# Kernel tuning notes

Measured on AMD Instinct MI355X. Metric: run time of the kernel, lower is better.

## Reference

```python
import jax, jax.numpy as jnp
import numpy as np

B, V = 4096, 50257          # batch, command-logit width
NUM_CAT, CMDS_PER_CAT = 8, 8
TOTAL_CMDS = NUM_CAT * CMDS_PER_CAT  # sum(len(cmds)) in source
TOPK = 5                    # min(5, V)
W_CMD, W_CAT = 0.6, 0.4     # hierarchy_weights


def setup_inputs() -> dict:
    key = jax.random.key(0)
    k1, k2, k3 = jax.random.split(key, 3)
    logits = jax.random.normal(k1, (B, V), dtype=jnp.float32)
    labels = jax.random.randint(k2, (B,), 0, V)
    category_labels = jax.random.randint(k3, (B,), 0, NUM_CAT)
    # precomputed command -> category index table (replaces python range search)
    cmd_to_cat = jnp.asarray(np.repeat(np.arange(NUM_CAT), CMDS_PER_CAT), dtype=jnp.int32)
    return {"logits": logits, "labels": labels,
            "category_labels": category_labels, "cmd_to_cat": cmd_to_cat}


def _cross_entropy(logits, labels):
    # mean NLL, matching torch.nn.CrossEntropyLoss defaults
    logp = jax.nn.log_softmax(logits, axis=-1)
    nll = -jnp.take_along_axis(logp, labels[:, None], axis=-1)[:, 0]
    return jnp.mean(nll)


def reference(logits, labels, category_labels, cmd_to_cat):
    command_loss = _cross_entropy(logits, labels)

    # _aggregate_category_logits, vectorized:
    # topk values are exactly logits[b, cmd_idx] gathered in the source loop
    vals, idx = jax.lax.top_k(logits, TOPK)          # [B, K]
    cat_idx = cmd_to_cat[idx % TOTAL_CMDS]           # [B, K] category bins
    b = jnp.arange(logits.shape[0])[:, None]          # [B, 1]
    category_logits = jnp.zeros((logits.shape[0], NUM_CAT), dtype=logits.dtype)
    category_logits = category_logits.at[b, cat_idx].add(vals)

    category_loss = _cross_entropy(category_logits, category_labels)
    return W_CMD * command_loss + W_CAT * category_loss
```

## Files before the change

kernel.cpp:

```cpp
#include <hip/hip_runtime.h>
#include <math.h>

#define TPB 256
#define NCAT 8
#define LOG2E  1.44269504088896f
#define LN2    0.69314718055994f
#define SHIFT  32.0f

__global__ __launch_bounds__(TPB) void hcl_row_kernel(
    const float* __restrict__ logits,
    const int*   __restrict__ labels,
    const int*   __restrict__ cat_labels,
    const int*   __restrict__ cmd_to_cat,
    float*       __restrict__ row_loss,
    int V)
{
    const int row  = blockIdx.x;
    const int tid  = threadIdx.x;
    const int lane = tid & 63;
    const int wave = tid >> 6;
    const float* __restrict__ rl = logits + (size_t)row * (size_t)V;

    float s0 = 0.0f, s1 = 0.0f, s2 = 0.0f, s3 = 0.0f;
    float v0=-INFINITY, v1=-INFINITY, v2=-INFINITY, v3=-INFINITY, v4=-INFINITY;
    int   i0=0, i1=0, i2=0, i3=0, i4=0;

#define INSERT(val, gidx) do {                                               \
        v4 = (val); i4 = (gidx);                                             \
        if (v4 > v3) { float t=v3; v3=v4; v4=t; int u=i3; i3=i4; i4=u; }     \
        if (v3 > v2) { float t=v2; v2=v3; v3=t; int u=i2; i2=i3; i3=u; }     \
        if (v2 > v1) { float t=v1; v1=v2; v2=t; int u=i1; i1=i2; i2=u; }     \
        if (v1 > v0) { float t=v0; v0=v1; v1=t; int u=i0; i0=i1; i1=u; }     \
    } while (0)

    const int mis = (int)(((size_t)rl >> 2) & 3);
    const int pre = (4 - mis) & 3;
    const int nb  = (V - pre) >> 2;
    const float4* __restrict__ body = (const float4*)(rl + pre);

    for (int i = tid; i < nb; i += TPB) {
        float4 q = body[i];
        int gi = pre + 4 * i;
        s0 += exp2f(__builtin_fmaf(q.x, LOG2E, -SHIFT));
        s1 += exp2f(__builtin_fmaf(q.y, LOG2E, -SHIFT));
        s2 += exp2f(__builtin_fmaf(q.z, LOG2E, -SHIFT));
        s3 += exp2f(__builtin_fmaf(q.w, LOG2E, -SHIFT));
        if (__builtin_expect(q.x > v4, 0)) INSERT(q.x, gi);
        if (__builtin_expect(q.y > v4, 0)) INSERT(q.y, gi + 1);
        if (__builtin_expect(q.z > v4, 0)) INSERT(q.z, gi + 2);
        if (__builtin_expect(q.w > v4, 0)) INSERT(q.w, gi + 3);
    }
    if (tid < pre) {
        float v = rl[tid];
        s0 += exp2f(__builtin_fmaf(v, LOG2E, -SHIFT));
        if (v > v4) INSERT(v, tid);
    }
    for (int gi = pre + 4 * nb + tid; gi < V; gi += TPB) {
        float v = rl[gi];
        s0 += exp2f(__builtin_fmaf(v, LOG2E, -SHIFT));
        if (v > v4) INSERT(v, gi);
    }
#undef INSERT

    float s = (s0 + s1) + (s2 + s3);
    #pragma unroll
    for (int off = 32; off > 0; off >>= 1) s += __shfl_down(s, off);

    __shared__ float sh_s[TPB/64];
    __shared__ float sh_cv[TPB/64];
    __shared__ int   sh_ci[TPB/64];
    __shared__ float sh_bv;
    __shared__ int   sh_bi;

    if (lane == 0) sh_s[wave] = s;

    float top_v[5]; int top_i[5];
    #pragma unroll
    for (int r = 0; r < 5; ++r) {
        float cv = v0; int ci = i0;
        #pragma unroll
        for (int off = 32; off > 0; off >>= 1) {
            float ov = __shfl_down(cv, off);
            int   oi = __shfl_down(ci, off);
            if (ov > cv || (ov == cv && oi < ci)) { cv = ov; ci = oi; }
        }
        if (lane == 0) { sh_cv[wave] = cv; sh_ci[wave] = ci; }
        __syncthreads();
        if (tid == 0) {
            float bv = sh_cv[0]; int bi = sh_ci[0];
            #pragma unroll
            for (int w = 1; w < TPB/64; ++w) {
                float ov = sh_cv[w]; int oi = sh_ci[w];
                if (ov > bv || (ov == bv && oi < bi)) { bv = ov; bi = oi; }
            }
            sh_bv = bv; sh_bi = bi;
            top_v[r] = bv; top_i[r] = bi;
        }
        __syncthreads();
        if (v0 == sh_bv && i0 == sh_bi) {
            v0=v1; i0=i1; v1=v2; i1=i2; v2=v3; i2=i3; v3=v4; i3=i4;
            v4=-INFINITY; i4=0;
        }
    }

    if (tid == 0) {
        float fs = 0.0f;
        #pragma unroll
        for (int w = 0; w < TPB/64; ++w) fs += sh_s[w];
        float lse = (log2f(fs) + SHIFT) * LN2;
        float nll_cmd = lse - rl[labels[row]];

        float cl[NCAT];
        #pragma unroll
        for (int c = 0; c < NCAT; ++c) cl[c] = 0.0f;
        #pragma unroll
        for (int r = 0; r < 5; ++r) {
            int c = cmd_to_cat[top_i[r] & 63];
            float v = top_v[r];
            #pragma unroll
            for (int k = 0; k < NCAT; ++k)
                cl[k] += (k == c) ? v : 0.0f;
        }
        float mc = cl[0];
        #pragma unroll
        for (int c = 1; c < NCAT; ++c) mc = fmaxf(mc, cl[c]);
        float se = 0.0f;
        #pragma unroll
        for (int c = 0; c < NCAT; ++c) se += __expf(cl[c] - mc);
        float lsec = mc + __logf(se);

        int clab = cat_labels[row];
        float tgt = 0.0f;
        #pragma unroll
        for (int c = 0; c < NCAT; ++c) tgt += (c == clab) ? cl[c] : 0.0f;
        float nll_cat = lsec - tgt;

        row_loss[row] = 0.6f * nll_cmd + 0.4f * nll_cat;
    }
}

__global__ __launch_bounds__(TPB) void hcl_reduce_kernel(
    const float* __restrict__ row_loss, float* __restrict__ out, int B)
{
    const int tid = threadIdx.x;
    float s = 0.0f;
    for (int i = tid; i < B; i += TPB) s += row_loss[i];
    #pragma unroll
    for (int off = 32; off > 0; off >>= 1) s += __shfl_down(s, off);
    __shared__ float sh[TPB/64];
    const int lane = tid & 63, wave = tid >> 6;
    if (lane == 0) sh[wave] = s;
    __syncthreads();
    if (tid == 0) {
        float t = 0.0f;
        #pragma unroll
        for (int w = 0; w < TPB/64; ++w) t += sh[w];
        out[0] = t / (float)B;
    }
}

extern "C" void kernel_launch(void* const* d_in, const int* in_sizes, int n_in,
                              void* d_out, int out_size, void* d_ws, size_t ws_size,
                              hipStream_t stream) {
    const float* logits     = (const float*)d_in[0];
    const int*   labels     = (const int*)  d_in[1];
    const int*   cat_labels = (const int*)  d_in[2];
    const int*   cmd_to_cat = (const int*)  d_in[3];
    const int B = in_sizes[1];
    const int V = in_sizes[0] / B;
    float* row_loss = (float*)d_ws;

    hcl_row_kernel<<<B, TPB, 0, stream>>>(logits, labels, cat_labels,
                                          cmd_to_cat, row_loss, V);
    hcl_reduce_kernel<<<1, TPB, 0, stream>>>(row_loss, (float*)d_out, B);
}
```

Measured before the change: 1.069 ms.

## Replace per-thread top-5 insertion with threshold-filtered shared candidate list

The main streaming loop no longer keeps a per-thread sorted top-5. Values above a fixed threshold are appended to a shared candidate buffer through an atomic counter, and a single wave then picks the top 5 from that buffer. If fewer than 5 or more than CAP candidates are found, the kernel falls back to rescanning the row with the old insertion method. The loop is also unrolled to two float4 loads per iteration with eight accumulators. This removes branchy insertion work from the hot loop, but it depends on the input distribution, since the threshold assumes standard-normal logits, and the fallback pays for a second full read of the row.

Measured after the change: 1.031 ms. 3.6% less time.

```diff
diff --git a/kernel.cpp b/kernel.cpp
--- a/kernel.cpp
+++ b/kernel.cpp
@@ -3,6 +3,8 @@
 
 #define TPB 256
 #define NCAT 8
+#define CAP 512
+#define TAU 3.0f
 #define LOG2E  1.44269504088896f
 #define LN2    0.69314718055994f
 #define SHIFT  32.0f
@@ -21,10 +23,101 @@
     const int wave = tid >> 6;
     const float* __restrict__ rl = logits + (size_t)row * (size_t)V;
 
-    float s0 = 0.0f, s1 = 0.0f, s2 = 0.0f, s3 = 0.0f;
-    float v0=-INFINITY, v1=-INFINITY, v2=-INFINITY, v3=-INFINITY, v4=-INFINITY;
-    int   i0=0, i1=0, i2=0, i3=0, i4=0;
-
+    __shared__ float cand_v[CAP];
+    __shared__ int   cand_i[CAP];
+    __shared__ int   s_cnt;
+    __shared__ float sh_s[TPB/64];
+    __shared__ float s_top_v[5];
+    __shared__ int   s_top_i[5];
+    __shared__ int   s_c2c[64];
+    __shared__ float sh_cv[TPB/64];
+    __shared__ int   sh_ci[TPB/64];
+    __shared__ float sh_bv;
+    __shared__ int   sh_bi;
+
+    if (tid == 0) s_cnt = 0;
+    if (tid < 64) s_c2c[tid] = cmd_to_cat[tid];
+
+    int lab = 0, clab = 0; float tgt = 0.0f;
+    if (tid == 0) { lab = labels[row]; clab = cat_labels[row]; tgt = rl[lab]; }
+    __syncthreads();
+
+    const int mis = (int)(((size_t)rl >> 2) & 3);
+    const int pre = (4 - mis) & 3;
+    const int nb  = (V - pre) >> 2;
+    const float4* __restrict__ body = (const float4*)(rl + pre);
+
+    float a0=0.f,a1=0.f,a2=0.f,a3=0.f,a4=0.f,a5=0.f,a6=0.f,a7=0.f;
+
+#define APPEND(val, gidx) do {                                               \
+        int _s = atomicAdd(&s_cnt, 1);                                       \
+        if (_s < CAP) { cand_v[_s] = (val); cand_i[_s] = (gidx); }           \
+    } while (0)
+
+    int i = tid;
+    for (; i + TPB < nb; i += 2*TPB) {
+        float4 x = body[i];
+        float4 y = body[i + TPB];
+        a0 += exp2f(__builtin_fmaf(x.x, LOG2E, -SHIFT));
+        a1 += exp2f(__builtin_fmaf(x.y, LOG2E, -SHIFT));
+        a2 += exp2f(__builtin_fmaf(x.z, LOG2E, -SHIFT));
+        a3 += exp2f(__builtin_fmaf(x.w, LOG2E, -SHIFT));
+        a4 += exp2f(__builtin_fmaf(y.x, LOG2E, -SHIFT));
+        a5 += exp2f(__builtin_fmaf(y.y, LOG2E, -SHIFT));
+        a6 += exp2f(__builtin_fmaf(y.z, LOG2E, -SHIFT));
+        a7 += exp2f(__builtin_fmaf(y.w, LOG2E, -SHIFT));
+        float mx = fmaxf(fmaxf(fmaxf(x.x, x.y), fmaxf(x.z, x.w)),
+                         fmaxf(fmaxf(y.x, y.y), fmaxf(y.z, y.w)));
+        if (__builtin_expect(mx > TAU, 0)) {
+            int gx = pre + 4 * i;
+            int gy = pre + 4 * (i + TPB);
+            if (x.x > TAU) APPEND(x.x, gx);
+            if (x.y > TAU) APPEND(x.y, gx + 1);
+            if (x.z > TAU) APPEND(x.z, gx + 2);
+            if (x.w > TAU) APPEND(x.w, gx + 3);
+            if (y.x > TAU) APPEND(y.x, gy);
+            if (y.y > TAU) APPEND(y.y, gy + 1);
+            if (y.z > TAU) APPEND(y.z, gy + 2);
+            if (y.w > TAU) APPEND(y.w, gy + 3);
+        }
+    }
+    for (; i < nb; i += TPB) {
+        float4 x = body[i];
+        a0 += exp2f(__builtin_fmaf(x.x, LOG2E, -SHIFT));
+        a1 += exp2f(__builtin_fmaf(x.y, LOG2E, -SHIFT));
+        a2 += exp2f(__builtin_fmaf(x.z, LOG2E, -SHIFT));
+        a3 += exp2f(__builtin_fmaf(x.w, LOG2E, -SHIFT));
+        float mx = fmaxf(fmaxf(x.x, x.y), fmaxf(x.z, x.w));
+        if (__builtin_expect(mx > TAU, 0)) {
+            int gx = pre + 4 * i;
+            if (x.x > TAU) APPEND(x.x, gx);
+            if (x.y > TAU) APPEND(x.y, gx + 1);
+            if (x.z > TAU) APPEND(x.z, gx + 2);
+            if (x.w > TAU) APPEND(x.w, gx + 3);
+        }
+    }
+    if (tid < pre) {
+        float v = rl[tid];
+        a0 += exp2f(__builtin_fmaf(v, LOG2E, -SHIFT));
+        if (v > TAU) APPEND(v, tid);
+    }
+    for (int g = pre + 4 * nb + tid; g < V; g += TPB) {
+        float v = rl[g];
+        a0 += exp2f(__builtin_fmaf(v, LOG2E, -SHIFT));
+        if (v > TAU) APPEND(v, g);
+    }
+#undef APPEND
+
+    float s = ((a0 + a1) + (a2 + a3)) + ((a4 + a5) + (a6 + a7));
+    #pragma unroll
+    for (int off = 32; off > 0; off >>= 1) s += __shfl_down(s, off);
+    if (lane == 0) sh_s[wave] = s;
+    __syncthreads();
+
+    const int cnt = s_cnt;
+    if (cnt < 5 || cnt > CAP) {
+        float v0=-INFINITY,v1=-INFINITY,v2=-INFINITY,v3=-INFINITY,v4=-INFINITY;
+        int   i0=0, i1=0, i2=0, i3=0, i4=0;
 #define INSERT(val, gidx) do {                                               \
         v4 = (val); i4 = (gidx);                                             \
         if (v4 > v3) { float t=v3; v3=v4; v4=t; int u=i3; i3=i4; i4=u; }     \
@@ -32,74 +125,59 @@
         if (v2 > v1) { float t=v1; v1=v2; v2=t; int u=i1; i1=i2; i2=u; }     \
         if (v1 > v0) { float t=v0; v0=v1; v1=t; int u=i0; i0=i1; i1=u; }     \
     } while (0)
-
-    const int mis = (int)(((size_t)rl >> 2) & 3);
-    const int pre = (4 - mis) & 3;
-    const int nb  = (V - pre) >> 2;
-    const float4* __restrict__ body = (const float4*)(rl + pre);
-
-    for (int i = tid; i < nb; i += TPB) {
-        float4 q = body[i];
-        int gi = pre + 4 * i;
-        s0 += exp2f(__builtin_fmaf(q.x, LOG2E, -SHIFT));
-        s1 += exp2f(__builtin_fmaf(q.y, LOG2E, -SHIFT));
-        s2 += exp2f(__builtin_fmaf(q.z, LOG2E, -SHIFT));
-        s3 += exp2f(__builtin_fmaf(q.w, LOG2E, -SHIFT));
-        if (__builtin_expect(q.x > v4, 0)) INSERT(q.x, gi);
-        if (__builtin_expect(q.y > v4, 0)) INSERT(q.y, gi + 1);
-        if (__builtin_expect(q.z > v4, 0)) INSERT(q.z, gi + 2);
-        if (__builtin_expect(q.w > v4, 0)) INSERT(q.w, gi + 3);
-    }
-    if (tid < pre) {
-        float v = rl[tid];
-        s0 += exp2f(__builtin_fmaf(v, LOG2E, -SHIFT));
-        if (v > v4) INSERT(v, tid);
-    }
-    for (int gi = pre + 4 * nb + tid; gi < V; gi += TPB) {
-        float v = rl[gi];
-        s0 += exp2f(__builtin_fmaf(v, LOG2E, -SHIFT));
-        if (v > v4) INSERT(v, gi);
-    }
+        for (int g = tid; g < V; g += TPB) {
+            float v = rl[g];
+            if (v > v4) INSERT(v, g);
+        }
 #undef INSERT
-
-    float s = (s0 + s1) + (s2 + s3);
-    #pragma unroll
-    for (int off = 32; off > 0; off >>= 1) s += __shfl_down(s, off);
-
-    __shared__ float sh_s[TPB/64];
-    __shared__ float sh_cv[TPB/64];
-    __shared__ int   sh_ci[TPB/64];
-    __shared__ float sh_bv;
-    __shared__ int   sh_bi;
-
-    if (lane == 0) sh_s[wave] = s;
-
-    float top_v[5]; int top_i[5];
-    #pragma unroll
-    for (int r = 0; r < 5; ++r) {
-        float cv = v0; int ci = i0;
-        #pragma unroll
-        for (int off = 32; off > 0; off >>= 1) {
-            float ov = __shfl_down(cv, off);
-            int   oi = __shfl_down(ci, off);
-            if (ov > cv || (ov == cv && oi < ci)) { cv = ov; ci = oi; }
-        }
-        if (lane == 0) { sh_cv[wave] = cv; sh_ci[wave] = ci; }
-        __syncthreads();
-        if (tid == 0) {
-            float bv = sh_cv[0]; int bi = sh_ci[0];
+        #pragma unroll
+        for (int r = 0; r < 5; ++r) {
+            float cv = v0; int ci = i0;
             #pragma unroll
-            for (int w = 1; w < TPB/64; ++w) {
-                float ov = sh_cv[w]; int oi = sh_ci[w];
-                if (ov > bv || (ov == bv && oi < bi)) { bv = ov; bi = oi; }
-            }
-            sh_bv = bv; sh_bi = bi;
-            top_v[r] = bv; top_i[r] = bi;
-        }
-        __syncthreads();
-        if (v0 == sh_bv && i0 == sh_bi) {
-            v0=v1; i0=i1; v1=v2; i1=i2; v2=v3; i2=i3; v3=v4; i3=i4;
-            v4=-INFINITY; i4=0;
+            for (int off = 32; off > 0; off >>= 1) {
+                float ov = __shfl_down(cv, off);
+                int   oi = __shfl_down(ci, off);
+                if (ov > cv || (ov == cv && oi < ci)) { cv = ov; ci = oi; }
+            }
+            if (lane == 0) { sh_cv[wave] = cv; sh_ci[wave] = ci; }
+            __syncthreads();
+            if (tid == 0) {
+                float bv = sh_cv[0]; int bi = sh_ci[0];
+                #pragma unroll
+                for (int w = 1; w < TPB/64; ++w) {
+                    float ov = sh_cv[w]; int oi = sh_ci[w];
+                    if (ov > bv || (ov == bv && oi < bi)) { bv = ov; bi = oi; }
+                }
+                sh_bv = bv; sh_bi = bi;
+                s_top_v[r] = bv; s_top_i[r] = bi;
+            }
+            __syncthreads();
+            if (v0 == sh_bv && i0 == sh_bi) {
+                v0=v1; i0=i1; v1=v2; i1=i2; v2=v3; i2=i3; v3=v4; i3=i4;
+                v4=-INFINITY; i4=0;
+            }
+        }
+    } else {
+        for (int r = 0; r < 5; ++r) {
+            if (wave == 0) {
+                float cv = -INFINITY; int ci = 0x7fffffff; int cs = 0;
+                for (int j = lane; j < cnt; j += 64) {
+                    float v = cand_v[j]; int ix = cand_i[j];
+                    if (v > cv || (v == cv && ix < ci)) { cv = v; ci = ix; cs = j; }
+                }
+                #pragma unroll
+                for (int off = 32; off > 0; off >>= 1) {
+                    float ov = __shfl_down(cv, off);
+                    int   oi = __shfl_down(ci, off);
+                    int   os = __shfl_down(cs, off);
+                    if (ov > cv || (ov == cv && oi < ci)) { cv = ov; ci = oi; cs = os; }
+                }
+                if (lane == 0) {
+                    s_top_v[r] = cv; s_top_i[r] = ci;
+                    cand_v[cs] = -INFINITY;
+                }
+            }
+            __syncthreads();
         }
     }
 
@@ -108,15 +186,15 @@
         #pragma unroll
         for (int w = 0; w < TPB/64; ++w) fs += sh_s[w];
         float lse = (log2f(fs) + SHIFT) * LN2;
-        float nll_cmd = lse - rl[labels[row]];
+        float nll_cmd = lse - tgt;
 
         float cl[NCAT];
         #pragma unroll
         for (int c = 0; c < NCAT; ++c) cl[c] = 0.0f;
         #pragma unroll
         for (int r = 0; r < 5; ++r) {
-            int c = cmd_to_cat[top_i[r] & 63];
-            float v = top_v[r];
+            int c = s_c2c[s_top_i[r] & 63];
+            float v = s_top_v[r];
             #pragma unroll
             for (int k = 0; k < NCAT; ++k)
                 cl[k] += (k == c) ? v : 0.0f;
@@ -129,11 +207,10 @@
         for (int c = 0; c < NCAT; ++c) se += __expf(cl[c] - mc);
         float lsec = mc + __logf(se);
 
-        int clab = cat_labels[row];
-        float tgt = 0.0f;
-        #pragma unroll
-        for (int c = 0; c < NCAT; ++c) tgt += (c == clab) ? cl[c] : 0.0f;
-        float nll_cat = lsec - tgt;
+        float t2 = 0.0f;
+        #pragma unroll
+        for (int c = 0; c < NCAT; ++c) t2 += (c == clab) ? cl[c] : 0.0f;
+        float nll_cat = lsec - t2;
 
         row_loss[row] = 0.6f * nll_cmd + 0.4f * nll_cat;
     }
```
